# Kernel optimization log

Hardware: AMD Instinct MI355X
Metric: run time of the kernel (lower is better)

## Reference

```python
import jax, jax.numpy as jnp
import numpy as np

EPS = 1e-6


def _build_cayley():
    # Blade ordering of the CEGNN CliffordAlgebra for Cl(3,0): combinations order
    # 1, e1, e2, e3, e12, e13, e23, e123. Metric (1,1,1) => e_k^2 = +1.
    blades = [(), (0,), (1,), (2,), (0, 1), (0, 2), (1, 2), (0, 1, 2)]
    index = {b: i for i, b in enumerate(blades)}
    cayley = np.zeros((8, 8, 8), dtype=np.float32)
    for i, a in enumerate(blades):
        for j, b in enumerate(blades):
            arr = list(a) + list(b)
            sign = 1
            # bubble sort, counting transpositions of anticommuting generators
            for p in range(len(arr)):
                for q in range(len(arr) - 1):
                    if arr[q] > arr[q + 1]:
                        arr[q], arr[q + 1] = arr[q + 1], arr[q]
                        sign = -sign
            # contract equal adjacent generators (e_k e_k = +1)
            out = []
            q = 0
            while q < len(arr):
                if q + 1 < len(arr) and arr[q] == arr[q + 1]:
                    q += 2
                else:
                    out.append(arr[q])
                    q += 1
            cayley[i, j, index[tuple(out)]] = sign
    return cayley


_CAYLEY = jnp.asarray(_build_cayley())  # (8, 8, 8)


def _mvlinear(x, W, b):
    # MVLinear(subspaces=False): channel mixing shared across blades,
    # bias embedded into the scalar (grade-0) blade only.
    y = jnp.einsum("bmi,nm->bni", x, W)
    return y.at[:, :, 0].add(b)


def setup_inputs() -> dict:
    key = jax.random.key(0)
    ks = jax.random.split(key, 7)
    B, Cin, Ch, Cout = 16384, 512, 512, 512
    s = 1.0 / np.sqrt(Cin)
    return {
        "vec1": jax.random.normal(ks[0], (B, Cin, 8), dtype=jnp.float32),
        "W_left": jax.random.normal(ks[1], (Ch, Cin), dtype=jnp.float32) * s,
        "b_left": jax.random.normal(ks[2], (Ch,), dtype=jnp.float32) * 0.01,
        "W_right": jax.random.normal(ks[3], (Ch, Cin), dtype=jnp.float32) * s,
        "b_right": jax.random.normal(ks[4], (Ch,), dtype=jnp.float32) * 0.01,
        "W_out": jax.random.normal(ks[5], (Cout, Ch), dtype=jnp.float32) * s,
        "b_out": jax.random.normal(ks[6], (Cout,), dtype=jnp.float32) * 0.01,
        "a_norm": jnp.ones((Cout,), dtype=jnp.float32),
    }


def reference(vec1, W_left, b_left, W_right, b_right, W_out, b_out, a_norm):
    vec_right = _mvlinear(vec1, W_right, b_right)   # (B, Ch, 8)
    vec_left = _mvlinear(vec1, W_left, b_left)      # (B, Ch, 8)
    # geometric product via the sparse Cayley table of Cl(3,0)
    gp = jnp.einsum("bmi,ijk,bmj->bmk", vec_left, _CAYLEY, vec_right)
    out = _mvlinear(gp, W_out, b_out)               # (B, Cout, 8)
    # MVLayerNorm: per-multivector quadratic-form norm (all-positive metric =>
    # sqrt of sum of squared blade coefficients), averaged over channels.
    norm = jnp.sqrt(jnp.sum(out * out, axis=-1, keepdims=True))  # (B, Cout, 1)
    norm = jnp.mean(norm, axis=1, keepdims=True) + EPS           # (B, 1, 1)
    return a_norm[None, :, None] * out / norm
```

## Files before the change

### kernel.cpp

```cpp
#include <hip/hip_runtime.h>
#include <cstdint>
#include <cstddef>

typedef _Float16 f16;
typedef __attribute__((ext_vector_type(8))) _Float16 f16x8;
typedef __attribute__((ext_vector_type(4))) _Float16 f16x4;
typedef __attribute__((ext_vector_type(4))) float f32x4;

#define MFMA_F16(a, b, c) __builtin_amdgcn_mfma_f32_16x16x32_f16((a), (b), (c), 0, 0, 0)

#define GL2LDS(gsrc, ldst)                                                  \
    __builtin_amdgcn_global_load_lds(                                        \
        (const __attribute__((address_space(1))) void*)(gsrc),               \
        (__attribute__((address_space(3))) void*)(ldst), 16, 0, 0)

#define WAITV(n) asm volatile("s_waitcnt vmcnt(" #n ")" ::: "memory")
#define BAR() __builtin_amdgcn_s_barrier()

#define SWZ(row) (((row) >> 1) & 3)


__global__ __launch_bounds__(256) void k0(const float* __restrict__ x,
                                          const float* __restrict__ wl,
                                          const float* __restrict__ wr,
                                          const float* __restrict__ wo,
                                          f16* __restrict__ wdst,
                                          f16* __restrict__ xt) {
    const int bid = blockIdx.x;
    if (bid >= 8192) {
        int i = (bid - 8192) * 256 + threadIdx.x;
        wdst[i]          = (f16)wl[i];
        wdst[262144 + i] = (f16)wr[i];
        wdst[524288 + i] = (f16)wo[i];
        return;
    }
    const int b = (bid >> 1) * 4 + (threadIdx.x >> 6);
    const int m = (bid & 1) * 256 + (threadIdx.x & 63) * 4;
    const float* src = x + ((size_t)b * 512 + m) * 8;
    f32x4 v[8];
#pragma unroll
    for (int u = 0; u < 8; ++u) v[u] = *(const f32x4*)(src + u * 4);
#pragma unroll
    for (int i = 0; i < 8; ++i) {
        f16x4 w;
#pragma unroll
        for (int j = 0; j < 4; ++j) w[j] = (f16)v[j * 2 + (i >> 2)][i & 3];
        *(f16x4*)(xt + (size_t)i * 8388608 + (size_t)b * 512 + m) = w;
    }
}

__global__ __launch_bounds__(512, 2) void k1(
    const f16* __restrict__ xt, const f16* __restrict__ wf,
    const float* __restrict__ bl_p, const float* __restrict__ br_p,
    char* gp_out)
{
    __shared__ __align__(16) f16 AsF[3 * 8192];
    __shared__ __align__(16) f16 WsF[3 * 4096];

    const int L = blockIdx.x;
    const int xcd = L & 7, sl = L >> 3;
    const int bt = xcd * 64 + (sl >> 3), ct = sl & 7;
    const int b0 = bt * 32, n0 = ct * 64;

    const int tid = threadIdx.x, lane = tid & 63, wv = tid >> 6;
    const int wb = wv >> 2, wn = wv & 3;
    const int r_lo = lane & 15, s_hi = lane >> 4;

    const int gA0 = tid, gA1 = tid + 512;
    const int ba0 = gA0 >> 7, ra0 = (gA0 >> 2) & 31, ga0 = (gA0 & 3) ^ SWZ(ra0);
    const int ba1 = gA1 >> 7, ra1 = (gA1 >> 2) & 31, ga1 = (gA1 & 3) ^ SWZ(ra1);
    const f16* aS0 = xt + (size_t)ba0 * 8388608 + (size_t)(b0 + ra0) * 512 + ga0 * 8;
    const f16* aS1 = xt + (size_t)ba1 * 8388608 + (size_t)(b0 + ra1) * 512 + ga1 * 8;
    const int side = tid >> 8, wn_ = (tid >> 2) & 63, wg = (tid & 3) ^ SWZ(wn_);
    const f16* wS = wf + (size_t)side * 262144 + (size_t)(n0 + wn_) * 512 + wg * 8;

    f16* aD0 = AsF + wv * 512;
    f16* aD1 = AsF + 4096 + wv * 512;
    f16* wD  = WsF + wv * 512;

    const int ar = wb * 16 + r_lo;
    const int aoff = ar * 32 + ((s_hi ^ SWZ(ar)) << 3);
    const int nloc = wn * 16 + r_lo;
    const int boff = nloc * 32 + ((s_hi ^ SWZ(nloc)) << 3);

    f32x4 accL[8], accR[8];
    const f32x4 zero = {0.f, 0.f, 0.f, 0.f};
#pragma unroll
    for (int i = 0; i < 8; ++i) { accL[i] = zero; accR[i] = zero; }

    auto stage = [&](int kt, int buf) {
        GL2LDS(aS0 + kt * 32, aD0 + buf * 8192);
        GL2LDS(aS1 + kt * 32, aD1 + buf * 8192);
        GL2LDS(wS + kt * 32, wD + buf * 4096);
    };

    stage(0, 0);
    stage(1, 1);

#pragma unroll
    for (int kk = 0; kk < 16; ++kk) {
        if (kk + 2 < 16) stage(kk + 2, (kk + 2) % 3);
        if (kk <= 13)      { WAITV(6); }
        else if (kk == 14) { WAITV(3); }
        else               { WAITV(0); }
        BAR();
        const f16* Ab = AsF + (kk % 3) * 8192;
        const f16* Wb = WsF + (kk % 3) * 4096;
        f16x8 bL = *(const f16x8*)(Wb + boff);
        f16x8 bR = *(const f16x8*)(Wb + 2048 + boff);
#pragma unroll
        for (int i = 0; i < 8; ++i) {
            f16x8 a = *(const f16x8*)(Ab + i * 1024 + aoff);
            accL[i] = MFMA_F16(a, bL, accL[i]);
            accR[i] = MFMA_F16(a, bR, accR[i]);
        }
        BAR();
    }

    const int n_g = n0 + nloc;
    const float blv = bl_p[n_g], brv = br_p[n_g];
#pragma unroll
    for (int rr = 0; rr < 4; ++rr) {
        const int b_g = b0 + wb * 16 + s_hi * 4 + rr;
        float Lv[8], Rv[8];
#pragma unroll
        for (int i = 0; i < 8; ++i) { Lv[i] = accL[i][rr]; Rv[i] = accR[i][rr]; }
        Lv[0] += blv; Rv[0] += brv;
        float g[8];
        g[0] = Lv[0]*Rv[0]+Lv[1]*Rv[1]+Lv[2]*Rv[2]+Lv[3]*Rv[3]-Lv[4]*Rv[4]-Lv[5]*Rv[5]-Lv[6]*Rv[6]-Lv[7]*Rv[7];
        g[1] = Lv[0]*Rv[1]+Lv[1]*Rv[0]-Lv[2]*Rv[4]-Lv[3]*Rv[5]+Lv[4]*Rv[2]+Lv[5]*Rv[3]-Lv[6]*Rv[7]-Lv[7]*Rv[6];
        g[2] = Lv[0]*Rv[2]+Lv[1]*Rv[4]+Lv[2]*Rv[0]-Lv[3]*Rv[6]-Lv[4]*Rv[1]+Lv[5]*Rv[7]+Lv[6]*Rv[3]+Lv[7]*Rv[5];
        g[3] = Lv[0]*Rv[3]+Lv[1]*Rv[5]+Lv[2]*Rv[6]+Lv[3]*Rv[0]-Lv[4]*Rv[7]-Lv[5]*Rv[1]-Lv[6]*Rv[2]-Lv[7]*Rv[4];
        g[4] = Lv[0]*Rv[4]+Lv[1]*Rv[2]-Lv[2]*Rv[1]+Lv[3]*Rv[7]+Lv[4]*Rv[0]-Lv[5]*Rv[6]+Lv[6]*Rv[5]+Lv[7]*Rv[3];
        g[5] = Lv[0]*Rv[5]+Lv[1]*Rv[3]-Lv[2]*Rv[7]-Lv[3]*Rv[1]+Lv[4]*Rv[6]+Lv[5]*Rv[0]-Lv[6]*Rv[4]-Lv[7]*Rv[2];
        g[6] = Lv[0]*Rv[6]+Lv[1]*Rv[7]+Lv[2]*Rv[3]-Lv[3]*Rv[2]-Lv[4]*Rv[5]+Lv[5]*Rv[4]+Lv[6]*Rv[0]+Lv[7]*Rv[1];
        g[7] = Lv[0]*Rv[7]+Lv[1]*Rv[6]-Lv[2]*Rv[5]+Lv[3]*Rv[4]+Lv[4]*Rv[3]-Lv[5]*Rv[2]+Lv[6]*Rv[1]+Lv[7]*Rv[0];
        char* dst = gp_out + (size_t)b_g * 16384 + (size_t)n_g * 2;
#pragma unroll
        for (int i = 0; i < 8; ++i) *(f16*)(dst + (size_t)i * 1024) = (f16)g[i];
    }
}

__global__ __launch_bounds__(512, 1) void k2(
    const char* gp_in, const f16* __restrict__ wo,
    const float* __restrict__ bo_p, const float* __restrict__ an_p,
    float* outp)
{
    __shared__ __align__(16) f16 AsF[3 * 4096];
    __shared__ __align__(16) f16 BsF[3 * 16384];
    __shared__ float red[16][8];

    const int b0 = blockIdx.x * 16;
    const int tid = threadIdx.x, lane = tid & 63, wv = tid >> 6;
    const int r_lo = lane & 15, s_hi = lane >> 4;

    const int abl = tid >> 6, arw = (tid >> 2) & 15, agp = (tid & 3) ^ SWZ(arw);
    const char* aS = gp_in + (size_t)(b0 + arw) * 16384 + abl * 1024 + agp * 16;
    const f16* bS[4];
#pragma unroll
    for (int j = 0; j < 4; ++j) {
        const int g = j * 512 + tid;
        const int bn = g >> 2, bg = (g & 3) ^ SWZ(bn);
        bS[j] = wo + (size_t)bn * 512 + bg * 8;
    }

    f16* aD = AsF + wv * 512;
    f16* bD = BsF + wv * 512;

    const int aoff = r_lo * 32 + ((s_hi ^ SWZ(r_lo)) << 3);
    int boffs[4];
#pragma unroll
    for (int t = 0; t < 4; ++t) {
        const int nl = wv * 64 + t * 16 + r_lo;
        boffs[t] = nl * 32 + ((s_hi ^ SWZ(nl)) << 3);
    }

    f32x4 acc[4][8];
    const f32x4 zero = {0.f, 0.f, 0.f, 0.f};
#pragma unroll
    for (int t = 0; t < 4; ++t)
#pragma unroll
        for (int i = 0; i < 8; ++i) acc[t][i] = zero;

    auto stage = [&](int kt, int buf) {
        GL2LDS(aS + kt * 64, aD + buf * 4096);
#pragma unroll
        for (int j = 0; j < 4; ++j)
            GL2LDS(bS[j] + kt * 32, bD + buf * 16384 + j * 4096);
    };

    stage(0, 0);
    stage(1, 1);

#pragma unroll
    for (int kk = 0; kk < 16; ++kk) {
        if (kk + 2 < 16) stage(kk + 2, (kk + 2) % 3);
        if (kk <= 13)      { WAITV(10); }
        else if (kk == 14) { WAITV(5); }
        else               { WAITV(0); }
        BAR();
        const f16* Ab = AsF + (kk % 3) * 4096;
        const f16* Bb = BsF + (kk % 3) * 16384;
        f16x8 bf[4];
#pragma unroll
        for (int t = 0; t < 4; ++t) bf[t] = *(const f16x8*)(Bb + boffs[t]);
#pragma unroll
        for (int i = 0; i < 8; ++i) {
            f16x8 a = *(const f16x8*)(Ab + i * 512 + aoff);
            acc[0][i] = MFMA_F16(a, bf[0], acc[0][i]);
            acc[1][i] = MFMA_F16(a, bf[1], acc[1][i]);
            acc[2][i] = MFMA_F16(a, bf[2], acc[2][i]);
            acc[3][i] = MFMA_F16(a, bf[3], acc[3][i]);
        }
        BAR();
    }

    float bo_t[4], an_t[4];
#pragma unroll
    for (int t = 0; t < 4; ++t) {
        const int c = wv * 64 + t * 16 + r_lo;
        bo_t[t] = bo_p[c]; an_t[t] = an_p[c];
    }

    float partial[4];
#pragma unroll
    for (int rr = 0; rr < 4; ++rr) {
        float sum = 0.f;
#pragma unroll
        for (int t = 0; t < 4; ++t) {
            float o = acc[t][0][rr] + bo_t[t];
            float ss = o * o;
#pragma unroll
            for (int i = 1; i < 8; ++i) ss += acc[t][i][rr] * acc[t][i][rr];
            sum += sqrtf(ss);
        }
        partial[rr] = sum;
    }
#pragma unroll
    for (int off = 1; off < 16; off <<= 1)
#pragma unroll
        for (int rr = 0; rr < 4; ++rr) partial[rr] += __shfl_xor(partial[rr], off);
    if (r_lo == 0)
#pragma unroll
        for (int rr = 0; rr < 4; ++rr) red[s_hi * 4 + rr][wv] = partial[rr];
    __syncthreads();

#pragma unroll
    for (int rr = 0; rr < 4; ++rr) {
        float tot = 0.f;
#pragma unroll
        for (int w = 0; w < 8; ++w) tot += red[s_hi * 4 + rr][w];
        const float inv = 1.0f / (tot * (1.0f / 512.0f) + 1e-6f);
        const int b_g = b0 + s_hi * 4 + rr;
        float* dst = outp + (size_t)b_g * 4096;
#pragma unroll
        for (int t = 0; t < 4; ++t) {
            const float sc = an_t[t] * inv;
            const int c = wv * 64 + t * 16 + r_lo;
            f32x4 v0, v1;
            v0[0] = (acc[t][0][rr] + bo_t[t]) * sc;
            v0[1] = acc[t][1][rr] * sc; v0[2] = acc[t][2][rr] * sc; v0[3] = acc[t][3][rr] * sc;
            v1[0] = acc[t][4][rr] * sc; v1[1] = acc[t][5][rr] * sc;
            v1[2] = acc[t][6][rr] * sc; v1[3] = acc[t][7][rr] * sc;
            *(f32x4*)(dst + (size_t)c * 8) = v0;
            *(f32x4*)(dst + (size_t)c * 8 + 4) = v1;
        }
    }
}

extern "C" void kernel_launch(void* const* d_in, const int* in_sizes, int n_in,
                              void* d_out, int out_size, void* d_ws, size_t ws_size,
                              hipStream_t stream) {
    const float* x  = (const float*)d_in[0];
    const float* wl = (const float*)d_in[1];
    const float* bl = (const float*)d_in[2];
    const float* wr = (const float*)d_in[3];
    const float* br = (const float*)d_in[4];
    const float* wo = (const float*)d_in[5];
    const float* bo = (const float*)d_in[6];
    const float* an = (const float*)d_in[7];
    f16* wf = (f16*)d_ws;
    f16* xt = wf + (1 << 20);

    hipLaunchKernelGGL(k0, dim3(9216), dim3(256), 0, stream, x, wl, wr, wo, wf, xt);
    hipLaunchKernelGGL(k1, dim3(4096), dim3(512), 0, stream, xt, wf, bl, br, (char*)d_out);
    hipLaunchKernelGGL(k2, dim3(1024), dim3(512), 0, stream,
                       (const char*)d_out, wf + 524288, bo, an, (float*)d_out);
}
```

Baseline: 432.4 us.

## Widen k1 channel tile, split K-step staging into halves, add MFMA priority

k1 now covers 128 output channels per block instead of 64, so each A tile from xt is loaded once for twice as many channels and the grid shrinks to 2048 blocks. In both k1 and k2 each K step runs in two halves: the second half's global-to-LDS prefetch is issued after the first barrier, spreading load traffic across the step. MFMA bursts are wrapped in s_setprio to favour the matrix work. k2's launch bound is raised to 2 blocks per CU, and the larger accumulator set in k1 adds register pressure that may cut occupancy.

```diff
diff --git a/kernel.cpp b/kernel.cpp
--- a/kernel.cpp
+++ b/kernel.cpp
@@ -16,6 +16,7 @@
 
 #define WAITV(n) asm volatile("s_waitcnt vmcnt(" #n ")" ::: "memory")
 #define BAR() __builtin_amdgcn_s_barrier()
+#define PRIO(n) __builtin_amdgcn_s_setprio(n)
 
 #define SWZ(row) (((row) >> 1) & 3)
 
@@ -55,12 +56,12 @@
     char* gp_out)
 {
     __shared__ __align__(16) f16 AsF[3 * 8192];
-    __shared__ __align__(16) f16 WsF[3 * 4096];
+    __shared__ __align__(16) f16 BsF[3 * 8192];
 
     const int L = blockIdx.x;
     const int xcd = L & 7, sl = L >> 3;
-    const int bt = xcd * 64 + (sl >> 3), ct = sl & 7;
-    const int b0 = bt * 32, n0 = ct * 64;
+    const int bt = xcd * 64 + (sl >> 2), ct = sl & 3;
+    const int b0 = bt * 32, n0 = ct * 128;
 
     const int tid = threadIdx.x, lane = tid & 63, wv = tid >> 6;
     const int wb = wv >> 2, wn = wv & 3;
@@ -71,77 +72,114 @@
     const int ba1 = gA1 >> 7, ra1 = (gA1 >> 2) & 31, ga1 = (gA1 & 3) ^ SWZ(ra1);
     const f16* aS0 = xt + (size_t)ba0 * 8388608 + (size_t)(b0 + ra0) * 512 + ga0 * 8;
     const f16* aS1 = xt + (size_t)ba1 * 8388608 + (size_t)(b0 + ra1) * 512 + ga1 * 8;
-    const int side = tid >> 8, wn_ = (tid >> 2) & 63, wg = (tid & 3) ^ SWZ(wn_);
-    const f16* wS = wf + (size_t)side * 262144 + (size_t)(n0 + wn_) * 512 + wg * 8;
-
-    f16* aD0 = AsF + wv * 512;
-    f16* aD1 = AsF + 4096 + wv * 512;
-    f16* wD  = WsF + wv * 512;
+    const int wch = tid >> 2, wg = (tid & 3) ^ SWZ(wch);
+    const f16* wS0 = wf + (size_t)(n0 + wch) * 512 + wg * 8;
+    const f16* wS1 = wS0 + 262144;
 
     const int ar = wb * 16 + r_lo;
-    const int aoff = ar * 32 + ((s_hi ^ SWZ(ar)) << 3);
-    const int nloc = wn * 16 + r_lo;
-    const int boff = nloc * 32 + ((s_hi ^ SWZ(nloc)) << 3);
-
-    f32x4 accL[8], accR[8];
+    const int arow = ar * 32 + ((s_hi ^ SWZ(ar)) << 3);
+    int bro[4];
+#pragma unroll
+    for (int t = 0; t < 4; ++t) {
+        const int nrow = ((t & 2) ? 128 : 0) + wn * 32 + (t & 1) * 16 + r_lo;
+        bro[t] = nrow * 32 + ((s_hi ^ SWZ(nrow)) << 3);
+    }
+
+    f32x4 acc[8][4];
     const f32x4 zero = {0.f, 0.f, 0.f, 0.f};
 #pragma unroll
-    for (int i = 0; i < 8; ++i) { accL[i] = zero; accR[i] = zero; }
-
-    auto stage = [&](int kt, int buf) {
-        GL2LDS(aS0 + kt * 32, aD0 + buf * 8192);
-        GL2LDS(aS1 + kt * 32, aD1 + buf * 8192);
-        GL2LDS(wS + kt * 32, wD + buf * 4096);
+    for (int i = 0; i < 8; ++i)
+#pragma unroll
+        for (int t = 0; t < 4; ++t) acc[i][t] = zero;
+
+    auto stageA = [&](int kt, int buf) {
+        GL2LDS(aS0 + kt * 32, AsF + buf * 8192 + wv * 512);
+        GL2LDS(aS1 + kt * 32, AsF + buf * 8192 + 4096 + wv * 512);
     };
-
-    stage(0, 0);
-    stage(1, 1);
-
-#pragma unroll
-    for (int kk = 0; kk < 16; ++kk) {
-        if (kk + 2 < 16) stage(kk + 2, (kk + 2) % 3);
-        if (kk <= 13)      { WAITV(6); }
-        else if (kk == 14) { WAITV(3); }
+    auto stageB = [&](int kt, int buf) {
+        GL2LDS(wS0 + kt * 32, BsF + buf * 8192 + wv * 512);
+        GL2LDS(wS1 + kt * 32, BsF + buf * 8192 + 4096 + wv * 512);
+    };
+
+    stageA(0, 0); stageB(0, 0);
+    stageA(1, 1); stageB(1, 1);
+
+#pragma unroll
+    for (int kt = 0; kt < 16; ++kt) {
+        const int buf = kt % 3, nbuf = (kt + 2) % 3;
+        const f16* Ab = AsF + buf * 8192;
+        const f16* Bb = BsF + buf * 8192;
+        if (kt < 14) stageA(kt + 2, nbuf);
+        if (kt <= 13)      { WAITV(6); }
+        else if (kt == 14) { WAITV(4); }
         else               { WAITV(0); }
         BAR();
-        const f16* Ab = AsF + (kk % 3) * 8192;
-        const f16* Wb = WsF + (kk % 3) * 4096;
-        f16x8 bL = *(const f16x8*)(Wb + boff);
-        f16x8 bR = *(const f16x8*)(Wb + 2048 + boff);
-#pragma unroll
-        for (int i = 0; i < 8; ++i) {
-            f16x8 a = *(const f16x8*)(Ab + i * 1024 + aoff);
-            accL[i] = MFMA_F16(a, bL, accL[i]);
-            accR[i] = MFMA_F16(a, bR, accR[i]);
-        }
-        BAR();
-    }
-
-    const int n_g = n0 + nloc;
-    const float blv = bl_p[n_g], brv = br_p[n_g];
-#pragma unroll
-    for (int rr = 0; rr < 4; ++rr) {
-        const int b_g = b0 + wb * 16 + s_hi * 4 + rr;
-        float Lv[8], Rv[8];
-#pragma unroll
-        for (int i = 0; i < 8; ++i) { Lv[i] = accL[i][rr]; Rv[i] = accR[i][rr]; }
-        Lv[0] += blv; Rv[0] += brv;
-        float g[8];
-        g[0] = Lv[0]*Rv[0]+Lv[1]*Rv[1]+Lv[2]*Rv[2]+Lv[3]*Rv[3]-Lv[4]*Rv[4]-Lv[5]*Rv[5]-Lv[6]*Rv[6]-Lv[7]*Rv[7];
-        g[1] = Lv[0]*Rv[1]+Lv[1]*Rv[0]-Lv[2]*Rv[4]-Lv[3]*Rv[5]+Lv[4]*Rv[2]+Lv[5]*Rv[3]-Lv[6]*Rv[7]-Lv[7]*Rv[6];
-        g[2] = Lv[0]*Rv[2]+Lv[1]*Rv[4]+Lv[2]*Rv[0]-Lv[3]*Rv[6]-Lv[4]*Rv[1]+Lv[5]*Rv[7]+Lv[6]*Rv[3]+Lv[7]*Rv[5];
-        g[3] = Lv[0]*Rv[3]+Lv[1]*Rv[5]+Lv[2]*Rv[6]+Lv[3]*Rv[0]-Lv[4]*Rv[7]-Lv[5]*Rv[1]-Lv[6]*Rv[2]-Lv[7]*Rv[4];
-        g[4] = Lv[0]*Rv[4]+Lv[1]*Rv[2]-Lv[2]*Rv[1]+Lv[3]*Rv[7]+Lv[4]*Rv[0]-Lv[5]*Rv[6]+Lv[6]*Rv[5]+Lv[7]*Rv[3];
-        g[5] = Lv[0]*Rv[5]+Lv[1]*Rv[3]-Lv[2]*Rv[7]-Lv[3]*Rv[1]+Lv[4]*Rv[6]+Lv[5]*Rv[0]-Lv[6]*Rv[4]-Lv[7]*Rv[2];
-        g[6] = Lv[0]*Rv[6]+Lv[1]*Rv[7]+Lv[2]*Rv[3]-Lv[3]*Rv[2]-Lv[4]*Rv[5]+Lv[5]*Rv[4]+Lv[6]*Rv[0]+Lv[7]*Rv[1];
-        g[7] = Lv[0]*Rv[7]+Lv[1]*Rv[6]-Lv[2]*Rv[5]+Lv[3]*Rv[4]+Lv[4]*Rv[3]-Lv[5]*Rv[2]+Lv[6]*Rv[1]+Lv[7]*Rv[0];
-        char* dst = gp_out + (size_t)b_g * 16384 + (size_t)n_g * 2;
-#pragma unroll
-        for (int i = 0; i < 8; ++i) *(f16*)(dst + (size_t)i * 1024) = (f16)g[i];
+        f16x8 bf[4];
+#pragma unroll
+        for (int t = 0; t < 4; ++t) bf[t] = *(const f16x8*)(Bb + bro[t]);
+        {
+            f16x8 a0 = *(const f16x8*)(Ab + 0 * 1024 + arow);
+            f16x8 a1 = *(const f16x8*)(Ab + 1 * 1024 + arow);
+            f16x8 a2 = *(const f16x8*)(Ab + 2 * 1024 + arow);
+            f16x8 a3 = *(const f16x8*)(Ab + 3 * 1024 + arow);
+            PRIO(1);
+#pragma unroll
+            for (int t = 0; t < 4; ++t) {
+                acc[0][t] = MFMA_F16(a0, bf[t], acc[0][t]);
+                acc[1][t] = MFMA_F16(a1, bf[t], acc[1][t]);
+                acc[2][t] = MFMA_F16(a2, bf[t], acc[2][t]);
+                acc[3][t] = MFMA_F16(a3, bf[t], acc[3][t]);
+            }
+            PRIO(0);
+        }
+        BAR();
+        if (kt < 14) stageB(kt + 2, nbuf);
+        {
+            f16x8 a4 = *(const f16x8*)(Ab + 4 * 1024 + arow);
+            f16x8 a5 = *(const f16x8*)(Ab + 5 * 1024 + arow);
+            f16x8 a6 = *(const f16x8*)(Ab + 6 * 1024 + arow);
+            f16x8 a7 = *(const f16x8*)(Ab + 7 * 1024 + arow);
+            PRIO(1);
+#pragma unroll
+            for (int t = 0; t < 4; ++t) {
+                acc[4][t] = MFMA_F16(a4, bf[t], acc[4][t]);
+                acc[5][t] = MFMA_F16(a5, bf[t], acc[5][t]);
+                acc[6][t] = MFMA_F16(a6, bf[t], acc[6][t]);
+                acc[7][t] = MFMA_F16(a7, bf[t], acc[7][t]);
+            }
+            PRIO(0);
+        }
+        BAR();
+    }
+
+#pragma unroll
+    for (int t = 0; t < 2; ++t) {
+        const int ch = n0 + wn * 32 + t * 16 + r_lo;
+        const float blv = bl_p[ch], brv = br_p[ch];
+#pragma unroll
+        for (int rr = 0; rr < 4; ++rr) {
+            const int b_g = b0 + wb * 16 + s_hi * 4 + rr;
+            float Lv[8], Rv[8];
+#pragma unroll
+            for (int i = 0; i < 8; ++i) { Lv[i] = acc[i][t][rr]; Rv[i] = acc[i][2 + t][rr]; }
+            Lv[0] += blv; Rv[0] += brv;
+            float g[8];
+            g[0] = Lv[0]*Rv[0]+Lv[1]*Rv[1]+Lv[2]*Rv[2]+Lv[3]*Rv[3]-Lv[4]*Rv[4]-Lv[5]*Rv[5]-Lv[6]*Rv[6]-Lv[7]*Rv[7];
+            g[1] = Lv[0]*Rv[1]+Lv[1]*Rv[0]-Lv[2]*Rv[4]-Lv[3]*Rv[5]+Lv[4]*Rv[2]+Lv[5]*Rv[3]-Lv[6]*Rv[7]-Lv[7]*Rv[6];
+            g[2] = Lv[0]*Rv[2]+Lv[1]*Rv[4]+Lv[2]*Rv[0]-Lv[3]*Rv[6]-Lv[4]*Rv[1]+Lv[5]*Rv[7]+Lv[6]*Rv[3]+Lv[7]*Rv[5];
+            g[3] = Lv[0]*Rv[3]+Lv[1]*Rv[5]+Lv[2]*Rv[6]+Lv[3]*Rv[0]-Lv[4]*Rv[7]-Lv[5]*Rv[1]-Lv[6]*Rv[2]-Lv[7]*Rv[4];
+            g[4] = Lv[0]*Rv[4]+Lv[1]*Rv[2]-Lv[2]*Rv[1]+Lv[3]*Rv[7]+Lv[4]*Rv[0]-Lv[5]*Rv[6]+Lv[6]*Rv[5]+Lv[7]*Rv[3];
+            g[5] = Lv[0]*Rv[5]+Lv[1]*Rv[3]-Lv[2]*Rv[7]-Lv[3]*Rv[1]+Lv[4]*Rv[6]+Lv[5]*Rv[0]-Lv[6]*Rv[4]-Lv[7]*Rv[2];
+            g[6] = Lv[0]*Rv[6]+Lv[1]*Rv[7]+Lv[2]*Rv[3]-Lv[3]*Rv[2]-Lv[4]*Rv[5]+Lv[5]*Rv[4]+Lv[6]*Rv[0]+Lv[7]*Rv[1];
+            g[7] = Lv[0]*Rv[7]+Lv[1]*Rv[6]-Lv[2]*Rv[5]+Lv[3]*Rv[4]+Lv[4]*Rv[3]-Lv[5]*Rv[2]+Lv[6]*Rv[1]+Lv[7]*Rv[0];
+            char* dst = gp_out + (size_t)b_g * 16384 + (size_t)ch * 2;
+#pragma unroll
+            for (int i = 0; i < 8; ++i) *(f16*)(dst + (size_t)i * 1024) = (f16)g[i];
+        }
     }
 }
 
-__global__ __launch_bounds__(512, 1) void k2(
+__global__ __launch_bounds__(512, 2) void k2(
     const char* gp_in, const f16* __restrict__ wo,
     const float* __restrict__ bo_p, const float* __restrict__ an_p,
     float* outp)
@@ -155,62 +193,78 @@
     const int r_lo = lane & 15, s_hi = lane >> 4;
 
     const int abl = tid >> 6, arw = (tid >> 2) & 15, agp = (tid & 3) ^ SWZ(arw);
-    const char* aS = gp_in + (size_t)(b0 + arw) * 16384 + abl * 1024 + agp * 16;
+    const char* aS = gp_in + (size_t)(b0 + arw) * 16384 + (size_t)abl * 1024 + agp * 16;
     const f16* bS[4];
 #pragma unroll
     for (int j = 0; j < 4; ++j) {
-        const int g = j * 512 + tid;
-        const int bn = g >> 2, bg = (g & 3) ^ SWZ(bn);
-        bS[j] = wo + (size_t)bn * 512 + bg * 8;
-    }
-
-    f16* aD = AsF + wv * 512;
-    f16* bD = BsF + wv * 512;
+        const int n = j * 128 + (tid >> 2);
+        bS[j] = wo + (size_t)n * 512 + ((tid & 3) ^ SWZ(n)) * 8;
+    }
 
     const int aoff = r_lo * 32 + ((s_hi ^ SWZ(r_lo)) << 3);
-    int boffs[4];
+    int bro[4];
 #pragma unroll
     for (int t = 0; t < 4; ++t) {
-        const int nl = wv * 64 + t * 16 + r_lo;
-        boffs[t] = nl * 32 + ((s_hi ^ SWZ(nl)) << 3);
-    }
-
-    f32x4 acc[4][8];
+        const int nrow = wv * 64 + t * 16 + r_lo;
+        bro[t] = nrow * 32 + ((s_hi ^ SWZ(nrow)) << 3);
+    }
+
+    f32x4 acc[8][4];
     const f32x4 zero = {0.f, 0.f, 0.f, 0.f};
 #pragma unroll
-    for (int t = 0; t < 4; ++t)
-#pragma unroll
-        for (int i = 0; i < 8; ++i) acc[t][i] = zero;
-
-    auto stage = [&](int kt, int buf) {
-        GL2LDS(aS + kt * 64, aD + buf * 4096);
-#pragma unroll
-        for (int j = 0; j < 4; ++j)
-            GL2LDS(bS[j] + kt * 32, bD + buf * 16384 + j * 4096);
+    for (int i = 0; i < 8; ++i)
+#pragma unroll
+        for (int t = 0; t < 4; ++t) acc[i][t] = zero;
+
+    auto stageB01 = [&](int kt, int buf) {
+        GL2LDS(bS[0] + kt * 32, BsF + buf * 16384 + 0 * 4096 + wv * 512);
+        GL2LDS(bS[1] + kt * 32, BsF + buf * 16384 + 1 * 4096 + wv * 512);
     };
-
-    stage(0, 0);
-    stage(1, 1);
-
-#pragma unroll
-    for (int kk = 0; kk < 16; ++kk) {
-        if (kk + 2 < 16) stage(kk + 2, (kk + 2) % 3);
-        if (kk <= 13)      { WAITV(10); }
-        else if (kk == 14) { WAITV(5); }
+    auto stageAB23 = [&](int kt, int buf) {
+        GL2LDS(aS + kt * 64, AsF + buf * 4096 + wv * 512);
+        GL2LDS(bS[2] + kt * 32, BsF + buf * 16384 + 2 * 4096 + wv * 512);
+        GL2LDS(bS[3] + kt * 32, BsF + buf * 16384 + 3 * 4096 + wv * 512);
+    };
+
+    stageB01(0, 0); stageAB23(0, 0);
+    stageB01(1, 1); stageAB23(1, 1);
+
+#pragma unroll
+    for (int kt = 0; kt < 16; ++kt) {
+        const int buf = kt % 3, nbuf = (kt + 2) % 3;
+        const f16* Ab = AsF + buf * 4096;
+        const f16* Bb = BsF + buf * 16384;
+        if (kt < 14) stageB01(kt + 2, nbuf);
+        if (kt <= 13)      { WAITV(7); }
+        else if (kt == 14) { WAITV(5); }
         else               { WAITV(0); }
         BAR();
-        const f16* Ab = AsF + (kk % 3) * 4096;
-        const f16* Bb = BsF + (kk % 3) * 16384;
-        f16x8 bf[4];
-#pragma unroll
-        for (int t = 0; t < 4; ++t) bf[t] = *(const f16x8*)(Bb + boffs[t]);
-#pragma unroll
-        for (int i = 0; i < 8; ++i) {
-            f16x8 a = *(const f16x8*)(Ab + i * 512 + aoff);
-            acc[0][i] = MFMA_F16(a, bf[0], acc[0][i]);
-            acc[1][i] = MFMA_F16(a, bf[1], acc[1][i]);
-            acc[2][i] = MFMA_F16(a, bf[2], acc[2][i]);
-            acc[3][i] = MFMA_F16(a, bf[3], acc[3][i]);
+        f16x8 af[8];
+#pragma unroll
+        for (int i = 0; i < 8; ++i) af[i] = *(const f16x8*)(Ab + i * 512 + aoff);
+        {
+            f16x8 b0f = *(const f16x8*)(Bb + bro[0]);
+            f16x8 b1f = *(const f16x8*)(Bb + bro[1]);
+            PRIO(1);
+#pragma unroll
+            for (int i = 0; i < 8; ++i) {
+                acc[i][0] = MFMA_F16(af[i], b0f, acc[i][0]);
+                acc[i][1] = MFMA_F16(af[i], b1f, acc[i][1]);
+            }
+            PRIO(0);
+        }
+        BAR();
+        if (kt < 14) stageAB23(kt + 2, nbuf);
+        {
+            f16x8 b2f = *(const f16x8*)(Bb + bro[2]);
+            f16x8 b3f = *(const f16x8*)(Bb + bro[3]);
+            PRIO(1);
+#pragma unroll
+            for (int i = 0; i < 8; ++i) {
+                acc[i][2] = MFMA_F16(af[i], b2f, acc[i][2]);
+                acc[i][3] = MFMA_F16(af[i], b3f, acc[i][3]);
+            }
+            PRIO(0);
         }
         BAR();
     }
@@ -228,10 +282,10 @@
         float sum = 0.f;
 #pragma unroll
         for (int t = 0; t < 4; ++t) {
-            float o = acc[t][0][rr] + bo_t[t];
+            float o = acc[0][t][rr] + bo_t[t];
             float ss = o * o;
 #pragma unroll
-            for (int i = 1; i < 8; ++i) ss += acc[t][i][rr] * acc[t][i][rr];
+            for (int i = 1; i < 8; ++i) ss += acc[i][t][rr] * acc[i][t][rr];
             sum += sqrtf(ss);
         }
         partial[rr] = sum;
@@ -258,10 +312,10 @@
             const float sc = an_t[t] * inv;
             const int c = wv * 64 + t * 16 + r_lo;
             f32x4 v0, v1;
-            v0[0] = (acc[t][0][rr] + bo_t[t]) * sc;
-            v0[1] = acc[t][1][rr] * sc; v0[2] = acc[t][2][rr] * sc; v0[3] = acc[t][3][rr] * sc;
-            v1[0] = acc[t][4][rr] * sc; v1[1] = acc[t][5][rr] * sc;
-            v1[2] = acc[t][6][rr] * sc; v1[3] = acc[t][7][rr] * sc;
+            v0[0] = (acc[0][t][rr] + bo_t[t]) * sc;
+            v0[1] = acc[1][t][rr] * sc; v0[2] = acc[2][t][rr] * sc; v0[3] = acc[3][t][rr] * sc;
+            v1[0] = acc[4][t][rr] * sc; v1[1] = acc[5][t][rr] * sc;
+            v1[2] = acc[6][t][rr] * sc; v1[3] = acc[7][t][rr] * sc;
             *(f32x4*)(dst + (size_t)c * 8) = v0;
             *(f32x4*)(dst + (size_t)c * 8 + 4) = v1;
         }
@@ -283,7 +337,7 @@
     f16* xt = wf + (1 << 20);
 
     hipLaunchKernelGGL(k0, dim3(9216), dim3(256), 0, stream, x, wl, wr, wo, wf, xt);
-    hipLaunchKernelGGL(k1, dim3(4096), dim3(512), 0, stream, xt, wf, bl, br, (char*)d_out);
+    hipLaunchKernelGGL(k1, dim3(2048), dim3(512), 0, stream, xt, wf, bl, br, (char*)d_out);
     hipLaunchKernelGGL(k2, dim3(1024), dim3(512), 0, stream,
                        (const char*)d_out, wf + 524288, bo, an, (float*)d_out);
 }
```

Result: faster. 408.1 us, median of 5 (-5.6%).
